# Kernel tuning notes

Hardware: AMD Instinct MI355X
Metric: run time of the kernel (lower is better)

## Reference

```python
import jax, jax.numpy as jnp
import numpy as np


def setup_inputs() -> dict:
    key = jax.random.key(0)
    k1, k2, k3, k4 = jax.random.split(key, 4)
    N, C, R, G = 524288, 256, 16, 512
    x = jax.random.normal(k1, (N, C), dtype=jnp.float32)
    segment_ids = jnp.sort(jax.random.randint(k2, (N,), 0, G)).astype(jnp.int64)
    # MLP params (Linear stores weight as [out,in] in torch; we keep [in,out] and matmul)
    W1 = jax.random.normal(k3, (C, C // R), dtype=jnp.float32) * (1.0 / np.sqrt(C))
    b1 = jnp.zeros((C // R,), dtype=jnp.float32)
    W2 = jax.random.normal(k4, (C // R, C), dtype=jnp.float32) * (1.0 / np.sqrt(C // R))
    b2 = jnp.zeros((C,), dtype=jnp.float32)
    return {"x": x, "segment_ids": segment_ids, "num_graphs": G,
            "W1": W1, "b1": b1, "W2": W2, "b2": b2}


def reference(x, segment_ids, num_graphs, W1, b1, W2, b2):
    # Per-graph avg pooling: segment sum / node counts. [G, C]
    sums = jax.ops.segment_sum(x, segment_ids, num_segments=num_graphs)
    counts = jax.ops.segment_sum(jnp.ones((x.shape[0],), dtype=x.dtype),
                                 segment_ids, num_segments=num_graphs)
    avg_pool = sums / jnp.maximum(counts, 1.0)[:, None]
    # Per-graph max pooling; guard empty segments (segment_max fills with -inf)
    max_pool = jax.ops.segment_max(x, segment_ids, num_segments=num_graphs)
    max_pool = jnp.where(counts[:, None] > 0, max_pool, 0.0)

    def mlp(p):
        return jax.nn.relu(p @ W1 + b1) @ W2 + b2

    channel_att = jax.nn.sigmoid(mlp(avg_pool) + mlp(max_pool))  # [G, C]
    # Broadcast each graph's attention vector to its nodes (segment gather)
    return x * channel_att[segment_ids]
```

## Files before the change

kernel.cpp:

```cpp
#include <hip/hip_runtime.h>
#include <cfloat>
#include <cmath>

#define CCH 256
#define HID 16

__global__ __launch_bounds__(512) void pool_mlp_kernel(
    const float* __restrict__ x, const int* __restrict__ seg,
    const int* __restrict__ numg,
    const float* __restrict__ W1, const float* __restrict__ b1,
    const float* __restrict__ W2, const float* __restrict__ b2,
    float* __restrict__ att, int N)
{
    const int G = *numg;
    const int tid = threadIdx.x;
    const int c4  = tid & 63;
    const int r   = tid >> 6;

    __shared__ float4 lsum[512];
    __shared__ float4 lmax[512];
    __shared__ float  avgp[CCH];
    __shared__ float  maxp[CCH];
    __shared__ float  ht[2 * HID];

    for (int g = (int)blockIdx.x; g < G; g += (int)gridDim.x) {
        int lo = 0, hi = N;
        while (lo < hi) { int mid = (lo + hi) >> 1; if (seg[mid] < g) lo = mid + 1; else hi = mid; }
        const int start = lo;
        hi = N;
        while (lo < hi) { int mid = (lo + hi) >> 1; if (seg[mid] < g + 1) lo = mid + 1; else hi = mid; }
        const int end = lo;
        const int count = end - start;

        float4 s = make_float4(0.f, 0.f, 0.f, 0.f);
        float4 m = make_float4(-FLT_MAX, -FLT_MAX, -FLT_MAX, -FLT_MAX);
        for (int n = start + r; n < end; n += 8) {
            const float4 v = *reinterpret_cast<const float4*>(x + (size_t)n * CCH + c4 * 4);
            s.x += v.x; s.y += v.y; s.z += v.z; s.w += v.w;
            m.x = fmaxf(m.x, v.x); m.y = fmaxf(m.y, v.y);
            m.z = fmaxf(m.z, v.z); m.w = fmaxf(m.w, v.w);
        }
        lsum[tid] = s; lmax[tid] = m;
        __syncthreads();

        if (tid < 64) {
            float4 S = lsum[tid];
            float4 M = lmax[tid];
            #pragma unroll
            for (int k = 1; k < 8; ++k) {
                const float4 S2 = lsum[tid + 64 * k];
                const float4 M2 = lmax[tid + 64 * k];
                S.x += S2.x; S.y += S2.y; S.z += S2.z; S.w += S2.w;
                M.x = fmaxf(M.x, M2.x); M.y = fmaxf(M.y, M2.y);
                M.z = fmaxf(M.z, M2.z); M.w = fmaxf(M.w, M2.w);
            }
            const float inv = (count > 0) ? 1.0f / (float)count : 0.0f;
            avgp[4 * tid + 0] = S.x * inv;
            avgp[4 * tid + 1] = S.y * inv;
            avgp[4 * tid + 2] = S.z * inv;
            avgp[4 * tid + 3] = S.w * inv;
            maxp[4 * tid + 0] = (count > 0) ? M.x : 0.0f;
            maxp[4 * tid + 1] = (count > 0) ? M.y : 0.0f;
            maxp[4 * tid + 2] = (count > 0) ? M.z : 0.0f;
            maxp[4 * tid + 3] = (count > 0) ? M.w : 0.0f;
        }
        __syncthreads();

        if (tid < 2 * HID) {
            const int j = tid & (HID - 1);
            const float* p = (tid < HID) ? avgp : maxp;
            float h = b1[j];
            #pragma unroll 4
            for (int c = 0; c < CCH; ++c) h = fmaf(p[c], W1[c * HID + j], h);
            ht[tid] = fmaxf(h, 0.0f);
        }
        __syncthreads();

        if (tid < CCH) {
            float acc = 2.0f * b2[tid];
            #pragma unroll
            for (int j = 0; j < HID; ++j)
                acc = fmaf(ht[j] + ht[HID + j], W2[j * CCH + tid], acc);
            att[(size_t)g * CCH + tid] = 1.0f / (1.0f + expf(-acc));
        }
        __syncthreads();
    }
}

__global__ __launch_bounds__(256) void apply_att_kernel(
    const float* __restrict__ x, const int* __restrict__ seg,
    const float* __restrict__ att, float* __restrict__ out, int n4)
{
    const int stride = (int)(gridDim.x * blockDim.x);
    for (int i = (int)(blockIdx.x * blockDim.x + threadIdx.x); i < n4; i += stride) {
        const int n = i >> 6;
        const int g = seg[n];
        const float4 a = reinterpret_cast<const float4*>(att)[(size_t)g * 64 + (i & 63)];
        const float4 v = reinterpret_cast<const float4*>(x)[i];
        float4 o;
        o.x = v.x * a.x; o.y = v.y * a.y; o.z = v.z * a.z; o.w = v.w * a.w;
        reinterpret_cast<float4*>(out)[i] = o;
    }
}

extern "C" void kernel_launch(void* const* d_in, const int* in_sizes, int n_in,
                              void* d_out, int out_size, void* d_ws, size_t ws_size,
                              hipStream_t stream) {
    const float* x    = (const float*)d_in[0];
    const int*   seg  = (const int*)d_in[1];
    const int*   numg = (const int*)d_in[2];
    const float* W1   = (const float*)d_in[3];
    const float* b1   = (const float*)d_in[4];
    const float* W2   = (const float*)d_in[5];
    const float* b2   = (const float*)d_in[6];
    float* out = (float*)d_out;
    float* att = (float*)d_ws;

    const int N = in_sizes[1];

    pool_mlp_kernel<<<512, 512, 0, stream>>>(x, seg, numg, W1, b1, W2, b2, att, N);

    const int n4 = out_size / 4;
    apply_att_kernel<<<2048, 256, 0, stream>>>(x, seg, att, out, n4);
}
```

Before: 338.1 us.

## Fuse pooling, MLP and attention apply into one per-segment kernel

Merges the pool+MLP kernel and the apply kernel so each block scales its own segment's rows right after computing attention, keeping attention in shared memory. The second pass walks the segment in reverse so recently read rows may still be in cache, and uses nontemporal stores for the output. The first-layer MLP is spread over all 512 threads with shuffle reductions, and the pooling loop is unrolled by two. The cost is that each block does its segment's pooling and apply back to back, with no overlap between the phases and no grid-wide load balancing in the apply step.

```diff
diff --git a/kernel.cpp b/kernel.cpp
--- a/kernel.cpp
+++ b/kernel.cpp
@@ -5,74 +5,93 @@
 #define CCH 256
 #define HID 16
 
-__global__ __launch_bounds__(512) void pool_mlp_kernel(
+typedef float f32x4 __attribute__((ext_vector_type(4)));
+
+__global__ __launch_bounds__(512) void fused_gca_kernel(
     const float* __restrict__ x, const int* __restrict__ seg,
     const int* __restrict__ numg,
     const float* __restrict__ W1, const float* __restrict__ b1,
     const float* __restrict__ W2, const float* __restrict__ b2,
-    float* __restrict__ att, int N)
+    float* __restrict__ out, int N)
 {
     const int G = *numg;
-    const int tid = threadIdx.x;
+    const int tid = (int)threadIdx.x;
     const int c4  = tid & 63;
     const int r   = tid >> 6;
 
-    __shared__ float4 lsum[512];
-    __shared__ float4 lmax[512];
-    __shared__ float  avgp[CCH];
-    __shared__ float  maxp[CCH];
-    __shared__ float  ht[2 * HID];
+    __shared__ f32x4 lsum[512];
+    __shared__ f32x4 lmax[512];
+    __shared__ float pool2[2 * CCH];
+    __shared__ float ht[2 * HID];
+    __shared__ float attn[CCH];
 
     for (int g = (int)blockIdx.x; g < G; g += (int)gridDim.x) {
         int lo = 0, hi = N;
         while (lo < hi) { int mid = (lo + hi) >> 1; if (seg[mid] < g) lo = mid + 1; else hi = mid; }
         const int start = lo;
         hi = N;
-        while (lo < hi) { int mid = (lo + hi) >> 1; if (seg[mid] < g + 1) lo = mid + 1; else hi = mid; }
+        while (lo < hi) { int mid = (lo + hi) >> 1; if (seg[mid] <= g) lo = mid + 1; else hi = mid; }
         const int end = lo;
         const int count = end - start;
 
-        float4 s = make_float4(0.f, 0.f, 0.f, 0.f);
-        float4 m = make_float4(-FLT_MAX, -FLT_MAX, -FLT_MAX, -FLT_MAX);
-        for (int n = start + r; n < end; n += 8) {
-            const float4 v = *reinterpret_cast<const float4*>(x + (size_t)n * CCH + c4 * 4);
-            s.x += v.x; s.y += v.y; s.z += v.z; s.w += v.w;
-            m.x = fmaxf(m.x, v.x); m.y = fmaxf(m.y, v.y);
-            m.z = fmaxf(m.z, v.z); m.w = fmaxf(m.w, v.w);
+        f32x4 s = {0.f, 0.f, 0.f, 0.f};
+        f32x4 m = {-FLT_MAX, -FLT_MAX, -FLT_MAX, -FLT_MAX};
+        int n = start + r;
+        for (; n + 8 < end; n += 16) {
+            const f32x4 v0 = *reinterpret_cast<const f32x4*>(x + (size_t)n * CCH + c4 * 4);
+            const f32x4 v1 = *reinterpret_cast<const f32x4*>(x + (size_t)(n + 8) * CCH + c4 * 4);
+            s += v0; s += v1;
+            m.x = fmaxf(fmaxf(m.x, v0.x), v1.x);
+            m.y = fmaxf(fmaxf(m.y, v0.y), v1.y);
+            m.z = fmaxf(fmaxf(m.z, v0.z), v1.z);
+            m.w = fmaxf(fmaxf(m.w, v0.w), v1.w);
+        }
+        if (n < end) {
+            const f32x4 v0 = *reinterpret_cast<const f32x4*>(x + (size_t)n * CCH + c4 * 4);
+            s += v0;
+            m.x = fmaxf(m.x, v0.x); m.y = fmaxf(m.y, v0.y);
+            m.z = fmaxf(m.z, v0.z); m.w = fmaxf(m.w, v0.w);
         }
         lsum[tid] = s; lmax[tid] = m;
         __syncthreads();
 
         if (tid < 64) {
-            float4 S = lsum[tid];
-            float4 M = lmax[tid];
+            f32x4 S = lsum[tid];
+            f32x4 M = lmax[tid];
             #pragma unroll
             for (int k = 1; k < 8; ++k) {
-                const float4 S2 = lsum[tid + 64 * k];
-                const float4 M2 = lmax[tid + 64 * k];
-                S.x += S2.x; S.y += S2.y; S.z += S2.z; S.w += S2.w;
+                const f32x4 S2 = lsum[tid + 64 * k];
+                const f32x4 M2 = lmax[tid + 64 * k];
+                S += S2;
                 M.x = fmaxf(M.x, M2.x); M.y = fmaxf(M.y, M2.y);
                 M.z = fmaxf(M.z, M2.z); M.w = fmaxf(M.w, M2.w);
             }
             const float inv = (count > 0) ? 1.0f / (float)count : 0.0f;
-            avgp[4 * tid + 0] = S.x * inv;
-            avgp[4 * tid + 1] = S.y * inv;
-            avgp[4 * tid + 2] = S.z * inv;
-            avgp[4 * tid + 3] = S.w * inv;
-            maxp[4 * tid + 0] = (count > 0) ? M.x : 0.0f;
-            maxp[4 * tid + 1] = (count > 0) ? M.y : 0.0f;
-            maxp[4 * tid + 2] = (count > 0) ? M.z : 0.0f;
-            maxp[4 * tid + 3] = (count > 0) ? M.w : 0.0f;
+            pool2[4 * tid + 0] = S.x * inv;
+            pool2[4 * tid + 1] = S.y * inv;
+            pool2[4 * tid + 2] = S.z * inv;
+            pool2[4 * tid + 3] = S.w * inv;
+            pool2[CCH + 4 * tid + 0] = (count > 0) ? M.x : 0.0f;
+            pool2[CCH + 4 * tid + 1] = (count > 0) ? M.y : 0.0f;
+            pool2[CCH + 4 * tid + 2] = (count > 0) ? M.z : 0.0f;
+            pool2[CCH + 4 * tid + 3] = (count > 0) ? M.w : 0.0f;
         }
         __syncthreads();
 
-        if (tid < 2 * HID) {
-            const int j = tid & (HID - 1);
-            const float* p = (tid < HID) ? avgp : maxp;
-            float h = b1[j];
-            #pragma unroll 4
-            for (int c = 0; c < CCH; ++c) h = fmaf(p[c], W1[c * HID + j], h);
-            ht[tid] = fmaxf(h, 0.0f);
+        {
+            const int pair = tid >> 4;
+            const int sub  = tid & 15;
+            const int j    = pair & (HID - 1);
+            const float* p = pool2 + (pair >> 4) * CCH;
+            float h = 0.f;
+            #pragma unroll
+            for (int c = sub; c < CCH; c += 16)
+                h = fmaf(p[c], W1[c * HID + j], h);
+            h += __shfl_xor(h, 8, 64);
+            h += __shfl_xor(h, 4, 64);
+            h += __shfl_xor(h, 2, 64);
+            h += __shfl_xor(h, 1, 64);
+            if (sub == 0) ht[pair] = fmaxf(h + b1[j], 0.0f);
         }
         __syncthreads();
 
@@ -81,25 +100,31 @@
             #pragma unroll
             for (int j = 0; j < HID; ++j)
                 acc = fmaf(ht[j] + ht[HID + j], W2[j * CCH + tid], acc);
-            att[(size_t)g * CCH + tid] = 1.0f / (1.0f + expf(-acc));
+            attn[tid] = 1.0f / (1.0f + expf(-acc));
         }
         __syncthreads();
-    }
-}
 
-__global__ __launch_bounds__(256) void apply_att_kernel(
-    const float* __restrict__ x, const int* __restrict__ seg,
-    const float* __restrict__ att, float* __restrict__ out, int n4)
-{
-    const int stride = (int)(gridDim.x * blockDim.x);
-    for (int i = (int)(blockIdx.x * blockDim.x + threadIdx.x); i < n4; i += stride) {
-        const int n = i >> 6;
-        const int g = seg[n];
-        const float4 a = reinterpret_cast<const float4*>(att)[(size_t)g * 64 + (i & 63)];
-        const float4 v = reinterpret_cast<const float4*>(x)[i];
-        float4 o;
-        o.x = v.x * a.x; o.y = v.y * a.y; o.z = v.z * a.z; o.w = v.w * a.w;
-        reinterpret_cast<float4*>(out)[i] = o;
+        {
+            const f32x4 a4 = *reinterpret_cast<const f32x4*>(attn + c4 * 4);
+            const int rem = end - (start + r);
+            if (rem > 0) {
+                int k = ((rem + 7) >> 3) - 1;
+                for (; k >= 1; k -= 2) {
+                    const size_t i0 = (size_t)(start + r + 8 * k) * CCH + c4 * 4;
+                    const size_t i1 = (size_t)(start + r + 8 * (k - 1)) * CCH + c4 * 4;
+                    const f32x4 v0 = *reinterpret_cast<const f32x4*>(x + i0);
+                    const f32x4 v1 = *reinterpret_cast<const f32x4*>(x + i1);
+                    __builtin_nontemporal_store(v0 * a4, reinterpret_cast<f32x4*>(out + i0));
+                    __builtin_nontemporal_store(v1 * a4, reinterpret_cast<f32x4*>(out + i1));
+                }
+                if (k == 0) {
+                    const size_t i0 = (size_t)(start + r) * CCH + c4 * 4;
+                    const f32x4 v0 = *reinterpret_cast<const f32x4*>(x + i0);
+                    __builtin_nontemporal_store(v0 * a4, reinterpret_cast<f32x4*>(out + i0));
+                }
+            }
+        }
+        __syncthreads();
     }
 }
 
@@ -114,12 +139,8 @@
     const float* W2   = (const float*)d_in[5];
     const float* b2   = (const float*)d_in[6];
     float* out = (float*)d_out;
-    float* att = (float*)d_ws;
 
     const int N = in_sizes[1];
 
-    pool_mlp_kernel<<<512, 512, 0, stream>>>(x, seg, numg, W1, b1, W2, b2, att, N);
-
-    const int n4 = out_size / 4;
-    apply_att_kernel<<<2048, 256, 0, stream>>>(x, seg, att, out, n4);
+    fused_gca_kernel<<<512, 512, 0, stream>>>(x, seg, numg, W1, b1, W2, b2, out, N);
 }
```

Result: faster. 284.9 us (-15.7%).
